# Kernel optimization log

Measured on AMD Instinct MI355X. Metric: run time of the kernel, lower is better.

Reference implementation:

```python
import jax, jax.numpy as jnp
import numpy as np

HIDDEN = 256


def setup_inputs() -> dict:
    key = jax.random.key(0)
    k1, k2, k3, k4, k5 = jax.random.split(key, 5)
    B, N, T, I, H = 64, 16, 128, 256, HIDDEN
    return {
        "x": jax.random.normal(k1, (B, N, T, I), dtype=jnp.float32),
        "weight_ih": jax.random.normal(k2, (1, N, 3 * H, I), dtype=jnp.float32) * 0.05,
        "weight_hh": jax.random.normal(k3, (1, N, 3 * H, H), dtype=jnp.float32) * 0.05,
        "bias_ih": jax.random.normal(k4, (1, N, 3 * H), dtype=jnp.float32) * 0.05,
        "bias_hh": jax.random.normal(k5, (1, N, 3 * H), dtype=jnp.float32) * 0.05,
    }


def _gru_scan(x, weight_ih, weight_hh, bias_ih, bias_hh):
    H = HIDDEN
    wih = weight_ih[0]  # [N, 3H, I]
    whh = weight_hh[0]  # [N, 3H, H]
    bih = bias_ih       # [1, N, 3H] broadcasts over batch
    bhh = bias_hh
    xt = jnp.transpose(x, (2, 0, 1, 3))  # [T, B, N, I]
    B, N = xt.shape[1], xt.shape[2]
    h0 = jnp.zeros((B, N, H), dtype=x.dtype)

    def step(h, x_t):
        ih = jnp.einsum('bni,ngi->bng', x_t, wih) + bih   # [B, N, 3H]
        hh = jnp.einsum('bnh,ngh->bng', h, whh) + bhh     # [B, N, 3H]
        rz = jax.nn.sigmoid(ih[..., :2 * H] + hh[..., :2 * H])
        r, z = rz[..., :H], rz[..., H:]
        n = jnp.tanh(ih[..., 2 * H:] + r * hh[..., 2 * H:])
        h_new = (1 - z) * n + z * h
        return h_new, h_new

    _, ys = jax.lax.scan(step, h0, xt)      # ys: [T, B, N, H]
    return jnp.transpose(ys, (1, 2, 0, 3))  # [B, N, T, H] (batch_first, output_num=-1)


def reference(x, weight_ih, weight_hh, bias_ih, bias_hh):
    return _gru_scan(x, weight_ih, weight_hh, bias_ih, bias_hh)
```

## Files before the change

kernel.cpp:

```cpp
#include <hip/hip_runtime.h>
#include <stdint.h>

#define B_ 64
#define N_ 16
#define T_ 128
#define I_ 256
#define H_ 256
#define G_ 768
#define TC 64

typedef __attribute__((ext_vector_type(8))) short bf8;
typedef __attribute__((ext_vector_type(8))) unsigned short u16x8;
typedef __attribute__((ext_vector_type(4))) float f4;

static __device__ __forceinline__ unsigned short f2bf(float f) {
    uint32_t u = __builtin_bit_cast(uint32_t, f);
    u += 0x7fffu + ((u >> 16) & 1u);
    return (unsigned short)(u >> 16);
}
static __device__ __forceinline__ float bf2f(unsigned short s) {
    return __builtin_bit_cast(float, ((uint32_t)s) << 16);
}
static __device__ __forceinline__ float sigm(float x) {
    return __builtin_amdgcn_rcpf(1.f + __expf(-x));
}

static __device__ __forceinline__ void barrier_lds_only() {
    asm volatile("s_waitcnt lgkmcnt(0)\n\ts_barrier" ::: "memory");
}

#define OFF_WIH   0ull
#define OFF_WHH   6291456ull
#define OFF_BIAS  12582912ull
#define OFF_H32   12632064ull
#define OFF_IH    13680640ull
#define WS_NEEDED (OFF_IH + 100663296ull)

__global__ __launch_bounds__(256) void prep_kernel(
        const float* __restrict__ wih, const float* __restrict__ whh,
        const float* __restrict__ bih, const float* __restrict__ bhh,
        unsigned char* ws) {
    unsigned short* wih_fr = (unsigned short*)(ws + OFF_WIH);
    unsigned short* whh_fr = (unsigned short*)(ws + OFF_WHH);
    float* bias_f = (float*)(ws + OFF_BIAS);
    int gid = blockIdx.x * blockDim.x + threadIdx.x;
    int nthr = gridDim.x * blockDim.x;

    for (int o = gid; o < 393216; o += nthr) {
        int lane = o & 63, kt = (o >> 6) & 7, ct = (o >> 9) % 48, n = o / 24576;
        int gcol = ct * 16 + (lane & 15);
        int k0 = kt * 32 + (lane >> 4) * 8;
        const float* s0 = wih + ((size_t)(n * G_ + gcol)) * I_ + k0;
        const float* s1 = whh + ((size_t)(n * G_ + gcol)) * H_ + k0;
        u16x8 v0, v1;
        #pragma unroll
        for (int e = 0; e < 8; e++) { v0[e] = f2bf(s0[e]); v1[e] = f2bf(s1[e]); }
        *(u16x8*)(wih_fr + (size_t)o * 8) = v0;
        *(u16x8*)(whh_fr + (size_t)o * 8) = v1;
    }
    for (int o = gid; o < N_ * G_; o += nthr) {
        int g = o % G_;
        bias_f[o] = bih[o] + (g < 512 ? bhh[o] : 0.f);
    }
}

__global__ __launch_bounds__(1024, 1) void ih_gemm(
        const float* __restrict__ x, const unsigned char* __restrict__ wsr,
        unsigned char* ws, int t0) {
    const unsigned short* wih_fr = (const unsigned short*)(wsr + OFF_WIH);
    const float* bias_f = (const float*)(wsr + OFF_BIAS);
    unsigned short* IH = (unsigned short*)(ws + OFF_IH);

    __shared__ __align__(16) unsigned short As[4 * 64 * 256];

    int tid = threadIdx.x, lane = tid & 63, w = tid >> 6;
    int blk = blockIdx.x;
    int n = (blk & 7) * 2 + (blk >> 7);
    int bq = (blk >> 3) & 15;
    int c16 = lane & 15, q = lane >> 4, q16 = q * 8;

    #pragma unroll
    for (int i = 0; i < 4; i++) {
        int b = bq * 4 + i;
        const float* xb = x + (((size_t)(b * N_ + n)) * T_ + t0) * I_;
        #pragma unroll
        for (int j = 0; j < 2; j++) {
            int chunk = j * 1024 + tid;
            int row = chunk >> 5, kc = chunk & 31;
            const float* s = xb + row * I_ + kc * 8;
            float4 f0 = *(const float4*)s;
            float4 f1 = *(const float4*)(s + 4);
            u16x8 v;
            v[0] = f2bf(f0.x); v[1] = f2bf(f0.y); v[2] = f2bf(f0.z); v[3] = f2bf(f0.w);
            v[4] = f2bf(f1.x); v[5] = f2bf(f1.y); v[6] = f2bf(f1.z); v[7] = f2bf(f1.w);
            int eoff = i * 16384 + row * 256 + ((kc * 8) ^ ((row & 7) << 3));
            *(u16x8*)(As + eoff) = v;
        }
    }
    __syncthreads();

    const unsigned short* bptr = wih_fr + (((size_t)n * 48 + w * 3) * 8) * 64 * 8;
    f4 zf = {0.f, 0.f, 0.f, 0.f};

    #pragma unroll 1
    for (int i = 0; i < 4; i++) {
        int b = bq * 4 + i;
        const unsigned short* Ai = As + i * 16384;

        f4 acc[4][3];
        #pragma unroll
        for (int rt = 0; rt < 4; rt++)
            #pragma unroll
            for (int c = 0; c < 3; c++) acc[rt][c] = zf;

        bf8 bc[3], bn[3];
        #pragma unroll
        for (int c = 0; c < 3; c++)
            bc[c] = *(const bf8*)(bptr + (((size_t)c * 8 + 0) * 64 + lane) * 8);

        #pragma unroll 1
        for (int kt = 0; kt < 8; kt++) {
            int ktn = (kt + 1) & 7;
            #pragma unroll
            for (int c = 0; c < 3; c++)
                bn[c] = *(const bf8*)(bptr + (((size_t)c * 8 + ktn) * 64 + lane) * 8);
            bf8 a[4];
            #pragma unroll
            for (int rt = 0; rt < 4; rt++) {
                int ar = rt * 16 + c16;
                a[rt] = *(const bf8*)(Ai + ar * 256 + ((kt * 32 + q16) ^ ((ar & 7) << 3)));
            }
            #pragma unroll
            for (int c = 0; c < 3; c++)
                #pragma unroll
                for (int rt = 0; rt < 4; rt++)
                    acc[rt][c] = __builtin_amdgcn_mfma_f32_16x16x32_bf16(a[rt], bc[c], acc[rt][c], 0, 0, 0);
            #pragma unroll
            for (int c = 0; c < 3; c++) bc[c] = bn[c];
        }

        unsigned short* ob = IH + (size_t)(b * N_ + n) * 49152 + lane;
        #pragma unroll
        for (int c = 0; c < 3; c++) {
            int ct = w * 3 + c;
            float bias = bias_f[n * G_ + ct * 16 + c16];
            #pragma unroll
            for (int rt = 0; rt < 4; rt++) {
                #pragma unroll
                for (int r = 0; r < 4; r++)
                    ob[(((rt * 48 + ct) * 4) + r) * 64] = f2bf(acc[rt][c][r] + bias);
            }
        }
    }
}

__global__ __launch_bounds__(512, 1) void gru_scan(
        const unsigned char* __restrict__ wsr, unsigned char* ws,
        const float* __restrict__ bhh, float* __restrict__ out,
        int chunk, int t0) {
    const unsigned short* IH = (const unsigned short*)(wsr + OFF_IH);
    const unsigned short* whh_fr = (const unsigned short*)(wsr + OFF_WHH);
    float* h32ws = (float*)(ws + OFF_H32);

    __shared__ __align__(16) unsigned short hbf[2][4][272];

    int tid = threadIdx.x, lane = tid & 63, w = tid >> 6;
    int n = blockIdx.x & 15, rg = blockIdx.x >> 4;

    int c16 = lane & 15;
    int q = lane >> 4;
    int hrow = c16 >> 2;
    int q16 = q * 8;
    int brow = rg * 4 + q;

    bf8 wf[3][2][8];
    #pragma unroll
    for (int g = 0; g < 3; g++)
        #pragma unroll
        for (int u = 0; u < 2; u++) {
            int ct = g * 16 + w * 2 + u;
            #pragma unroll
            for (int kt = 0; kt < 8; kt++)
                wf[g][u][kt] = *(const bf8*)(whh_fr + ((((size_t)n * 48 + ct) * 8 + kt) * 64 + lane) * 8);
        }

    int colb = w * 32 + c16;
    float bn0 = bhh[n * G_ + 512 + colb];
    float bn1 = bhh[n * G_ + 512 + colb + 16];
    float h0 = 0.f, h1 = 0.f;
    if (chunk) {
        const float* hp = h32ws + ((size_t)brow * N_ + n) * H_ + colb;
        h0 = hp[0]; h1 = hp[16];
    }
    hbf[0][q][colb] = f2bf(h0);
    hbf[0][q][colb + 16] = f2bf(h1);

    const unsigned short* ihb = IH + (size_t)(brow * N_ + n) * 49152 + c16;
    int cb2 = w * 512;

    #define TPART(t) (((t) >> 4) * 12288 + ((t) & 3) * 64 + (((t) >> 2) & 3) * 16)

    unsigned short c_r0, c_r1, c_z0, c_z1, c_n0, c_n1;
    {
        const unsigned short* p = ihb + TPART(0) + cb2;
        c_r0 = p[0];    c_r1 = p[256];
        c_z0 = p[4096]; c_z1 = p[4352];
        c_n0 = p[8192]; c_n1 = p[8448];
    }

    f4 zf = {0.f, 0.f, 0.f, 0.f};
    __syncthreads();

    #pragma unroll 1
    for (int t = 0; t < TC; t++) {
        int tn = (t + 1 < TC) ? (t + 1) : t;
        const unsigned short* p = ihb + TPART(tn) + cb2;
        unsigned short n_r0 = p[0],    n_r1 = p[256];
        unsigned short n_z0 = p[4096], n_z1 = p[4352];
        unsigned short n_n0 = p[8192], n_n1 = p[8448];

        const unsigned short* hb = &hbf[t & 1][0][0];
        f4 acc[3][2];
        #pragma unroll
        for (int g = 0; g < 3; g++)
            #pragma unroll
            for (int u = 0; u < 2; u++) acc[g][u] = zf;
        #pragma unroll
        for (int kt = 0; kt < 8; kt++) {
            bf8 a = *(const bf8*)(hb + hrow * 272 + kt * 32 + q16);
            #pragma unroll
            for (int g = 0; g < 3; g++)
                #pragma unroll
                for (int u = 0; u < 2; u++)
                    acc[g][u] = __builtin_amdgcn_mfma_f32_16x16x32_bf16(a, wf[g][u][kt], acc[g][u], 0, 0, 0);
        }

        float xr0 = bf2f(c_r0) + acc[0][0][0];
        float xz0 = bf2f(c_z0) + acc[1][0][0];
        float rr0 = sigm(xr0), zz0 = sigm(xz0);
        float pre0 = bf2f(c_n0) + rr0 * (acc[2][0][0] + bn0);
        float e20 = __expf(2.f * pre0);
        float nv0 = 1.f - 2.f * __builtin_amdgcn_rcpf(e20 + 1.f);
        float hn0 = nv0 + zz0 * (h0 - nv0);

        float xr1 = bf2f(c_r1) + acc[0][1][0];
        float xz1 = bf2f(c_z1) + acc[1][1][0];
        float rr1 = sigm(xr1), zz1 = sigm(xz1);
        float pre1 = bf2f(c_n1) + rr1 * (acc[2][1][0] + bn1);
        float e21 = __expf(2.f * pre1);
        float nv1 = 1.f - 2.f * __builtin_amdgcn_rcpf(e21 + 1.f);
        float hn1 = nv1 + zz1 * (h1 - nv1);

        h0 = hn0; h1 = hn1;

        unsigned short* hw = &hbf[(t & 1) ^ 1][q][colb];
        hw[0] = f2bf(hn0);
        hw[16] = f2bf(hn1);

        float* op = out + ((size_t)(brow * N_ + n) * T_ + (t0 + t)) * H_ + colb;
        op[0] = hn0;
        op[16] = hn1;

        c_r0 = n_r0; c_r1 = n_r1;
        c_z0 = n_z0; c_z1 = n_z1;
        c_n0 = n_n0; c_n1 = n_n1;

        barrier_lds_only();
    }

    float* hp = h32ws + ((size_t)brow * N_ + n) * H_ + colb;
    hp[0] = h0;
    hp[16] = h1;
}

extern "C" void kernel_launch(void* const* d_in, const int* in_sizes, int n_in,
                              void* d_out, int out_size, void* d_ws, size_t ws_size,
                              hipStream_t stream) {
    const float* x   = (const float*)d_in[0];
    const float* wih = (const float*)d_in[1];
    const float* whh = (const float*)d_in[2];
    const float* bih = (const float*)d_in[3];
    const float* bhh = (const float*)d_in[4];
    float* out = (float*)d_out;
    unsigned char* ws = (unsigned char*)d_ws;

    if (ws_size < WS_NEEDED) return;

    prep_kernel<<<1024, 256, 0, stream>>>(wih, whh, bih, bhh, ws);
    for (int chunk = 0; chunk < 2; chunk++) {
        int t0 = chunk * TC;
        ih_gemm<<<dim3(256), 1024, 0, stream>>>(x, ws, ws, t0);
        gru_scan<<<dim3(256), 512, 0, stream>>>(ws, ws, bhh, out, chunk, t0);
    }
}
```

Before: 271.7 us.

## Double-buffer x tiles in ih_gemm and remap gru_scan block indexing

The ih_gemm kernel stops staging all four batch rows of x into LDS up front. It now uses a two-slot LDS buffer and prefetches the next batch's x tile from global memory during the current tile's MFMA loop. The loads are split around the k-loop, then converted and stored after the output write, with a barrier per iteration. This cuts LDS use and overlaps global loads with compute. The register prefetch of weight fragments is dropped, and gru_scan's block-to-(n,rg) mapping is changed to match ih_gemm's ordering, presumably for cache or XCD locality.

```diff
diff --git a/kernel.cpp b/kernel.cpp
--- a/kernel.cpp
+++ b/kernel.cpp
@@ -23,6 +23,12 @@
 }
 static __device__ __forceinline__ float sigm(float x) {
     return __builtin_amdgcn_rcpf(1.f + __expf(-x));
+}
+static __device__ __forceinline__ u16x8 cvtu(float4 u, float4 v) {
+    u16x8 r;
+    r[0] = f2bf(u.x); r[1] = f2bf(u.y); r[2] = f2bf(u.z); r[3] = f2bf(u.w);
+    r[4] = f2bf(v.x); r[5] = f2bf(v.y); r[6] = f2bf(v.z); r[7] = f2bf(v.w);
+    return r;
 }
 
 static __device__ __forceinline__ void barrier_lds_only() {
@@ -71,7 +77,7 @@
     const float* bias_f = (const float*)(wsr + OFF_BIAS);
     unsigned short* IH = (unsigned short*)(ws + OFF_IH);
 
-    __shared__ __align__(16) unsigned short As[4 * 64 * 256];
+    __shared__ __align__(16) unsigned short As[2][64 * 256];
 
     int tid = threadIdx.x, lane = tid & 63, w = tid >> 6;
     int blk = blockIdx.x;
@@ -79,23 +85,18 @@
     int bq = (blk >> 3) & 15;
     int c16 = lane & 15, q = lane >> 4, q16 = q * 8;
 
-    #pragma unroll
-    for (int i = 0; i < 4; i++) {
-        int b = bq * 4 + i;
-        const float* xb = x + (((size_t)(b * N_ + n)) * T_ + t0) * I_;
-        #pragma unroll
-        for (int j = 0; j < 2; j++) {
-            int chunk = j * 1024 + tid;
-            int row = chunk >> 5, kc = chunk & 31;
-            const float* s = xb + row * I_ + kc * 8;
-            float4 f0 = *(const float4*)s;
-            float4 f1 = *(const float4*)(s + 4);
-            u16x8 v;
-            v[0] = f2bf(f0.x); v[1] = f2bf(f0.y); v[2] = f2bf(f0.z); v[3] = f2bf(f0.w);
-            v[4] = f2bf(f1.x); v[5] = f2bf(f1.y); v[6] = f2bf(f1.z); v[7] = f2bf(f1.w);
-            int eoff = i * 16384 + row * 256 + ((kc * 8) ^ ((row & 7) << 3));
-            *(u16x8*)(As + eoff) = v;
-        }
+    int rowj0 = tid >> 5, rowj1 = 32 + (tid >> 5), kc = tid & 31;
+    size_t off0 = (size_t)rowj0 * I_ + kc * 8;
+    size_t off1 = (size_t)rowj1 * I_ + kc * 8;
+    int e0 = rowj0 * 256 + ((kc * 8) ^ ((rowj0 & 7) << 3));
+    int e1 = rowj1 * 256 + ((kc * 8) ^ ((rowj1 & 7) << 3));
+
+    {
+        const float* xb = x + (((size_t)((bq * 4) * N_ + n)) * T_ + t0) * I_;
+        float4 a0 = *(const float4*)(xb + off0), a1 = *(const float4*)(xb + off0 + 4);
+        float4 b0 = *(const float4*)(xb + off1), b1 = *(const float4*)(xb + off1 + 4);
+        *(u16x8*)(&As[0][0] + e0) = cvtu(a0, a1);
+        *(u16x8*)(&As[0][0] + e1) = cvtu(b0, b1);
     }
     __syncthreads();
 
@@ -105,25 +106,28 @@
     #pragma unroll 1
     for (int i = 0; i < 4; i++) {
         int b = bq * 4 + i;
-        const unsigned short* Ai = As + i * 16384;
+        const unsigned short* Ai = &As[i & 1][0];
+        unsigned short* An = &As[(i + 1) & 1][0];
+        const float* xbn = x + (((size_t)((b + 1) * N_ + n)) * T_ + t0) * I_;
+
+        float4 p00, p01, p10, p11;
+        if (i < 3) {
+            p00 = *(const float4*)(xbn + off0);
+            p01 = *(const float4*)(xbn + off0 + 4);
+        }
 
         f4 acc[4][3];
         #pragma unroll
         for (int rt = 0; rt < 4; rt++)
             #pragma unroll
             for (int c = 0; c < 3; c++) acc[rt][c] = zf;
-
-        bf8 bc[3], bn[3];
-        #pragma unroll
-        for (int c = 0; c < 3; c++)
-            bc[c] = *(const bf8*)(bptr + (((size_t)c * 8 + 0) * 64 + lane) * 8);
 
         #pragma unroll 1
         for (int kt = 0; kt < 8; kt++) {
-            int ktn = (kt + 1) & 7;
+            bf8 bb[3];
             #pragma unroll
             for (int c = 0; c < 3; c++)
-                bn[c] = *(const bf8*)(bptr + (((size_t)c * 8 + ktn) * 64 + lane) * 8);
+                bb[c] = *(const bf8*)(bptr + (((size_t)c * 8 + kt) * 64 + lane) * 8);
             bf8 a[4];
             #pragma unroll
             for (int rt = 0; rt < 4; rt++) {
@@ -134,9 +138,11 @@
             for (int c = 0; c < 3; c++)
                 #pragma unroll
                 for (int rt = 0; rt < 4; rt++)
-                    acc[rt][c] = __builtin_amdgcn_mfma_f32_16x16x32_bf16(a[rt], bc[c], acc[rt][c], 0, 0, 0);
-            #pragma unroll
-            for (int c = 0; c < 3; c++) bc[c] = bn[c];
+                    acc[rt][c] = __builtin_amdgcn_mfma_f32_16x16x32_bf16(a[rt], bb[c], acc[rt][c], 0, 0, 0);
+            if (kt == 3 && i < 3) {
+                p10 = *(const float4*)(xbn + off1);
+                p11 = *(const float4*)(xbn + off1 + 4);
+            }
         }
 
         unsigned short* ob = IH + (size_t)(b * N_ + n) * 49152 + lane;
@@ -151,6 +157,12 @@
                     ob[(((rt * 48 + ct) * 4) + r) * 64] = f2bf(acc[rt][c][r] + bias);
             }
         }
+
+        if (i < 3) {
+            *(u16x8*)(An + e0) = cvtu(p00, p01);
+            *(u16x8*)(An + e1) = cvtu(p10, p11);
+        }
+        barrier_lds_only();
     }
 }
 
@@ -165,7 +177,9 @@
     __shared__ __align__(16) unsigned short hbf[2][4][272];
 
     int tid = threadIdx.x, lane = tid & 63, w = tid >> 6;
-    int n = blockIdx.x & 15, rg = blockIdx.x >> 4;
+    int blk = blockIdx.x;
+    int n = (blk & 7) * 2 + (blk >> 7);
+    int rg = (blk >> 3) & 15;
 
     int c16 = lane & 15;
     int q = lane >> 4;
```

After: 276.7 us. Within noise of the previous version (+1.9%).

## Split GRU scan across 16 waves with one column tile each

Applied to the files above, without the earlier changes.

The recurrent scan block grows from 8 to 16 waves, so each wave owns a single 16-column tile per gate instead of two. Per-step MFMA chain length and gate math per wave are halved, which shortens the serial critical path of each timestep and halves weight registers per thread. The next-step IH prefetch is dropped and loads now happen inline. Barrier cost rises with twice as many waves, and only one block fits per CU.

```diff
diff --git a/kernel.cpp b/kernel.cpp
--- a/kernel.cpp
+++ b/kernel.cpp
@@ -154,7 +154,7 @@
     }
 }
 
-__global__ __launch_bounds__(512, 1) void gru_scan(
+__global__ __launch_bounds__(1024, 1) void gru_scan(
         const unsigned char* __restrict__ wsr, unsigned char* ws,
         const float* __restrict__ bhh, float* __restrict__ out,
         int chunk, int t0) {
@@ -172,105 +172,62 @@
     int hrow = c16 >> 2;
     int q16 = q * 8;
     int brow = rg * 4 + q;
-
-    bf8 wf[3][2][8];
+    int col = w * 16 + c16;
+
+    bf8 wf[3][8];
     #pragma unroll
-    for (int g = 0; g < 3; g++)
-        #pragma unroll
-        for (int u = 0; u < 2; u++) {
-            int ct = g * 16 + w * 2 + u;
-            #pragma unroll
-            for (int kt = 0; kt < 8; kt++)
-                wf[g][u][kt] = *(const bf8*)(whh_fr + ((((size_t)n * 48 + ct) * 8 + kt) * 64 + lane) * 8);
-        }
-
-    int colb = w * 32 + c16;
-    float bn0 = bhh[n * G_ + 512 + colb];
-    float bn1 = bhh[n * G_ + 512 + colb + 16];
-    float h0 = 0.f, h1 = 0.f;
-    if (chunk) {
-        const float* hp = h32ws + ((size_t)brow * N_ + n) * H_ + colb;
-        h0 = hp[0]; h1 = hp[16];
-    }
-    hbf[0][q][colb] = f2bf(h0);
-    hbf[0][q][colb + 16] = f2bf(h1);
-
-    const unsigned short* ihb = IH + (size_t)(brow * N_ + n) * 49152 + c16;
-    int cb2 = w * 512;
+    for (int g = 0; g < 3; g++) {
+        int ct = g * 16 + w;
+        #pragma unroll
+        for (int kt = 0; kt < 8; kt++)
+            wf[g][kt] = *(const bf8*)(whh_fr + ((((size_t)n * 48 + ct) * 8 + kt) * 64 + lane) * 8);
+    }
+
+    float bn_hh = bhh[n * G_ + 512 + col];
+    float h = 0.f;
+    if (chunk) h = h32ws[((size_t)brow * N_ + n) * H_ + col];
+    hbf[0][q][col] = f2bf(h);
+
+    const unsigned short* ihb = IH + (size_t)(brow * N_ + n) * 49152 + w * 256 + c16;
+    float* op = out + ((size_t)(brow * N_ + n) * T_ + t0) * H_ + col;
 
     #define TPART(t) (((t) >> 4) * 12288 + ((t) & 3) * 64 + (((t) >> 2) & 3) * 16)
-
-    unsigned short c_r0, c_r1, c_z0, c_z1, c_n0, c_n1;
-    {
-        const unsigned short* p = ihb + TPART(0) + cb2;
-        c_r0 = p[0];    c_r1 = p[256];
-        c_z0 = p[4096]; c_z1 = p[4352];
-        c_n0 = p[8192]; c_n1 = p[8448];
-    }
 
     f4 zf = {0.f, 0.f, 0.f, 0.f};
     __syncthreads();
 
     #pragma unroll 1
     for (int t = 0; t < TC; t++) {
-        int tn = (t + 1 < TC) ? (t + 1) : t;
-        const unsigned short* p = ihb + TPART(tn) + cb2;
-        unsigned short n_r0 = p[0],    n_r1 = p[256];
-        unsigned short n_z0 = p[4096], n_z1 = p[4352];
-        unsigned short n_n0 = p[8192], n_n1 = p[8448];
+        const unsigned short* p = ihb + TPART(t);
+        unsigned short vr = p[0], vz = p[4096], vn = p[8192];
 
         const unsigned short* hb = &hbf[t & 1][0][0];
-        f4 acc[3][2];
-        #pragma unroll
-        for (int g = 0; g < 3; g++)
-            #pragma unroll
-            for (int u = 0; u < 2; u++) acc[g][u] = zf;
+        f4 acc0 = zf, acc1 = zf, acc2 = zf;
         #pragma unroll
         for (int kt = 0; kt < 8; kt++) {
             bf8 a = *(const bf8*)(hb + hrow * 272 + kt * 32 + q16);
-            #pragma unroll
-            for (int g = 0; g < 3; g++)
-                #pragma unroll
-                for (int u = 0; u < 2; u++)
-                    acc[g][u] = __builtin_amdgcn_mfma_f32_16x16x32_bf16(a, wf[g][u][kt], acc[g][u], 0, 0, 0);
-        }
-
-        float xr0 = bf2f(c_r0) + acc[0][0][0];
-        float xz0 = bf2f(c_z0) + acc[1][0][0];
-        float rr0 = sigm(xr0), zz0 = sigm(xz0);
-        float pre0 = bf2f(c_n0) + rr0 * (acc[2][0][0] + bn0);
-        float e20 = __expf(2.f * pre0);
-        float nv0 = 1.f - 2.f * __builtin_amdgcn_rcpf(e20 + 1.f);
-        float hn0 = nv0 + zz0 * (h0 - nv0);
-
-        float xr1 = bf2f(c_r1) + acc[0][1][0];
-        float xz1 = bf2f(c_z1) + acc[1][1][0];
-        float rr1 = sigm(xr1), zz1 = sigm(xz1);
-        float pre1 = bf2f(c_n1) + rr1 * (acc[2][1][0] + bn1);
-        float e21 = __expf(2.f * pre1);
-        float nv1 = 1.f - 2.f * __builtin_amdgcn_rcpf(e21 + 1.f);
-        float hn1 = nv1 + zz1 * (h1 - nv1);
-
-        h0 = hn0; h1 = hn1;
-
-        unsigned short* hw = &hbf[(t & 1) ^ 1][q][colb];
-        hw[0] = f2bf(hn0);
-        hw[16] = f2bf(hn1);
-
-        float* op = out + ((size_t)(brow * N_ + n) * T_ + (t0 + t)) * H_ + colb;
-        op[0] = hn0;
-        op[16] = hn1;
-
-        c_r0 = n_r0; c_r1 = n_r1;
-        c_z0 = n_z0; c_z1 = n_z1;
-        c_n0 = n_n0; c_n1 = n_n1;
+            acc0 = __builtin_amdgcn_mfma_f32_16x16x32_bf16(a, wf[0][kt], acc0, 0, 0, 0);
+            acc1 = __builtin_amdgcn_mfma_f32_16x16x32_bf16(a, wf[1][kt], acc1, 0, 0, 0);
+            acc2 = __builtin_amdgcn_mfma_f32_16x16x32_bf16(a, wf[2][kt], acc2, 0, 0, 0);
+        }
+
+        float xr = bf2f(vr) + acc0[0];
+        float xz = bf2f(vz) + acc1[0];
+        float rr = sigm(xr), zz = sigm(xz);
+        float pre = bf2f(vn) + rr * (acc2[0] + bn_hh);
+        float e2 = __expf(2.f * pre);
+        float nv = 1.f - 2.f * __builtin_amdgcn_rcpf(e2 + 1.f);
+        float hn = nv + zz * (h - nv);
+        h = hn;
+
+        hbf[(t & 1) ^ 1][q][col] = f2bf(hn);
+        *op = hn;
+        op += H_;
 
         barrier_lds_only();
     }
 
-    float* hp = h32ws + ((size_t)brow * N_ + n) * H_ + colb;
-    hp[0] = h0;
-    hp[16] = h1;
+    h32ws[((size_t)brow * N_ + n) * H_ + col] = h;
 }
 
 extern "C" void kernel_launch(void* const* d_in, const int* in_sizes, int n_in,
@@ -290,6 +247,6 @@
     for (int chunk = 0; chunk < 2; chunk++) {
         int t0 = chunk * TC;
         ih_gemm<<<dim3(256), 1024, 0, stream>>>(x, ws, ws, t0);
-        gru_scan<<<dim3(256), 512, 0, stream>>>(ws, ws, bhh, out, chunk, t0);
-    }
-}
+        gru_scan<<<dim3(256), 1024, 0, stream>>>(ws, ws, bhh, out, chunk, t0);
+    }
+}
```

New measurement: 287.4 us. 5.8% more time.
